# Performance work log

Measured on AMD Instinct MI355X. Metric: run time of the kernel, lower is better.

## Reference

```python
import jax, jax.numpy as jnp
import numpy as np

B, S, H = 64, 512, 768
BETA = 1.0
SENT_W, TOK_W, REG_W = 1.0, 1.0, 0.01


def setup_inputs() -> dict:
    key = jax.random.key(0)
    ks = jax.random.split(key, 8)
    hidden_states = jax.random.normal(ks[0], (B, S, H), dtype=jnp.float32)
    # offset_mapping[:,:,0] != 0 marks continuation subwords; position 0 is always a word start
    is_cont = jax.random.bernoulli(ks[1], 0.3, (B, S)).astype(jnp.int32)
    is_cont = is_cont.at[:, 0].set(0)
    offset_mapping = jnp.stack([is_cont, jnp.zeros((B, S), jnp.int32)], axis=-1)
    labels = jax.random.randint(ks[2], (B, S), 0, 2, dtype=jnp.int32)
    std = 0.02
    w1 = jax.random.normal(ks[3], (H, 100), jnp.float32) * std
    b1 = jnp.zeros((100,), jnp.float32)
    w2 = jax.random.normal(ks[4], (100, 1), jnp.float32) * std
    b2 = jnp.zeros((1,), jnp.float32)
    sw1 = jax.random.normal(ks[5], (H, 300), jnp.float32) * std
    sb1 = jnp.zeros((300,), jnp.float32)
    sw2 = jax.random.normal(ks[6], (300, 1), jnp.float32) * std
    sb2 = jnp.zeros((1,), jnp.float32)
    return dict(hidden_states=hidden_states, offset_mapping=offset_mapping, labels=labels,
                w1=w1, b1=b1, w2=w2, b2=b2, sw1=sw1, sb1=sb1, sw2=sw2, sb2=sb2)


def reference(hidden_states, offset_mapping, labels, w1, b1, w2, b2, sw1, sb1, sw2, sb2):
    b, s, h = hidden_states.shape
    # token attention head: Linear -> tanh -> Linear -> sigmoid, squeeze last dim
    tok = jax.nn.sigmoid(jnp.tanh(hidden_states @ w1 + b1) @ w2 + b2)[..., 0]  # [B,S]
    # vectorized segmented max over subword groups (replaces the python loop):
    # each word = a start position (offset[...,0]==0) plus following continuations.
    is_start = offset_mapping[:, :, 0] == 0  # [B,S]
    word_id = jnp.cumsum(is_start.astype(jnp.int32), axis=1) - 1  # per-row word index
    seg = (jnp.arange(b, dtype=jnp.int32)[:, None] * s + word_id).reshape(-1)  # global segment id
    segmax = jax.ops.segment_max(tok.reshape(-1), seg, num_segments=b * s)
    word_att = jnp.where(is_start, segmax[seg].reshape(b, s), tok)
    labf = labels.astype(tok.dtype)
    token_attention_mask = ((labels == 0) | (labels == 1)).astype(tok.dtype) * is_start.astype(tok.dtype)
    masked = word_att * token_attention_mask  # token_logits
    pw = jnp.power(masked, BETA)
    norm = pw / jnp.sum(pw, axis=1, keepdims=True)
    pooled = jnp.einsum('bsh,bs->bh', hidden_states, norm)  # bmm(hidden^T, att)
    sent = jax.nn.sigmoid(jnp.tanh(pooled @ sw1 + sb1) @ sw2 + sb2)  # [B,1] sequence_logits
    sentence_labels = jnp.max(labf, axis=1, keepdims=True)
    sentence_loss = jnp.sum((sent - sentence_labels) ** 2)
    zero_labels = jnp.where(labf == 1.0, labf, jnp.zeros_like(labf))
    token_loss = jnp.sum((masked - zero_labels) ** 2)
    ones_mask = jnp.where(masked == 0.0, jnp.ones_like(masked), masked)
    reg_a = jnp.sum(jnp.min(ones_mask, axis=1, keepdims=True) ** 2)
    reg_b = jnp.sum((jnp.max(masked, axis=1, keepdims=True) - sentence_labels) ** 2)
    loss = SENT_W * sentence_loss + TOK_W * token_loss + REG_W * (reg_a + reg_b)
    return loss, sentence_loss, token_loss, reg_a, reg_b, masked, sent
```

## Files before the change

kernel.cpp:

```cpp
#include <hip/hip_runtime.h>
#include <math.h>

#define BB   64
#define SS   512
#define HH   768
#define NU   100
#define NUP  112
#define NT   7
#define KS   24
#define NS1  300
#define MM   (BB*SS)
#define PCH  16
#define PTOK (SS/PCH)
#define UB   5
#define UPW  15

typedef __attribute__((ext_vector_type(8))) short short8;
typedef __attribute__((ext_vector_type(4))) float f32x4;

__device__ __forceinline__ unsigned short f2bf(float x) {
    unsigned int u = __float_as_uint(x);
    u = (u + 0x7FFFu + ((u >> 16) & 1u)) >> 16;
    return (unsigned short)u;
}

__device__ __forceinline__ float tanh_fast(float x) {
    float e = __expf(2.0f * x);
    return 1.0f - 2.0f / (e + 1.0f);
}

__device__ __forceinline__ float sigmoid_fast(float z) {
    return 1.0f / (1.0f + __expf(-z));
}

__global__ __launch_bounds__(64) void repack_kernel(
    const float* __restrict__ w1,
    const float* __restrict__ b1,
    const float* __restrict__ w2,
    const float* __restrict__ sw1,
    unsigned short* __restrict__ Bp,
    float* __restrict__ b1p, float* __restrict__ w2p,
    float* __restrict__ sw1T,
    float* __restrict__ accs,
    float* __restrict__ zacc,
    int*   __restrict__ btick)
{
    const int blk = blockIdx.x;
    const int l   = threadIdx.x;

    if (blk < NT * KS) {
        const int n  = blk / KS;
        const int ks = blk - n * KS;
        const int c  = l & 15, g = l >> 4;
        const int u  = n * 16 + c;

        unsigned int w[4];
#pragma unroll
        for (int jp = 0; jp < 4; jp++) {
            unsigned int lo, hi;
            {
                int k = ks * 32 + g * 8 + jp * 2;
                float x = (u < NU) ? w1[(size_t)k * NU + u] : 0.0f;
                lo = f2bf(x);
            }
            {
                int k = ks * 32 + g * 8 + jp * 2 + 1;
                float x = (u < NU) ? w1[(size_t)k * NU + u] : 0.0f;
                hi = f2bf(x);
            }
            w[jp] = lo | (hi << 16);
        }
        uint4* dst = (uint4*)(Bp + ((size_t)(n * KS + ks) * 64 + l) * 8);
        *dst = make_uint4(w[0], w[1], w[2], w[3]);

        if (blk == 0) {
            for (int i = l; i < NUP; i += 64) {
                b1p[i] = (i < NU) ? b1[i] : 0.0f;
                w2p[i] = (i < NU) ? w2[i] : 0.0f;
            }
            if (l < 8) accs[l] = 0.0f;
            zacc[l]  = 0.0f;
            btick[l] = 0;
        }
    } else {
        const int u = blk - NT * KS;
#pragma unroll
        for (int k = 0; k < HH / 64; k++) {
            int h = k * 64 + l;
            sw1T[(size_t)u * HH + h] = sw1[(size_t)h * NS1 + u];
        }
    }
}

__global__ __launch_bounds__(256) void tok_mlp_mfma(
    const float* __restrict__ hs,
    const unsigned short* __restrict__ Bp,
    const float* __restrict__ b1p,
    const float* __restrict__ w2p,
    const float* __restrict__ b2,
    float* __restrict__ tok)
{
    const int tid = threadIdx.x;
    const int wv = tid >> 6, l = tid & 63;
    const int c = l & 15, g = l >> 4;
    const int m0 = blockIdx.x * 64 + wv * 16;

    f32x4 acc[NT];
#pragma unroll
    for (int n = 0; n < NT; n++) acc[n] = (f32x4){0.f, 0.f, 0.f, 0.f};

    const float* arow = hs + (size_t)(m0 + c) * HH + g * 8;
    const unsigned short* bbase = Bp + (size_t)l * 8;

    float4 a0 = *(const float4*)(arow);
    float4 a1 = *(const float4*)(arow + 4);

    for (int ks = 0; ks < KS; ks++) {
        float4 n0 = a0, n1 = a1;
        if (ks + 1 < KS) {
            n0 = *(const float4*)(arow + (ks + 1) * 32);
            n1 = *(const float4*)(arow + (ks + 1) * 32 + 4);
        }
        short8 af;
        af[0] = (short)f2bf(a0.x); af[1] = (short)f2bf(a0.y);
        af[2] = (short)f2bf(a0.z); af[3] = (short)f2bf(a0.w);
        af[4] = (short)f2bf(a1.x); af[5] = (short)f2bf(a1.y);
        af[6] = (short)f2bf(a1.z); af[7] = (short)f2bf(a1.w);
#pragma unroll
        for (int n = 0; n < NT; n++) {
            short8 bf = *(const short8*)(bbase + (size_t)(n * KS + ks) * 64 * 8);
            acc[n] = __builtin_amdgcn_mfma_f32_16x16x32_bf16(af, bf, acc[n], 0, 0, 0);
        }
        a0 = n0; a1 = n1;
    }

    float p[4];
#pragma unroll
    for (int j = 0; j < 4; j++) {
        float s = 0.0f;
#pragma unroll
        for (int n = 0; n < NT; n++) {
            int u = n * 16 + c;
            s += tanh_fast(acc[n][j] + b1p[u]) * w2p[u];
        }
        p[j] = s;
    }
#pragma unroll
    for (int off = 1; off < 16; off <<= 1) {
#pragma unroll
        for (int j = 0; j < 4; j++) p[j] += __shfl_xor(p[j], off, 64);
    }
    if (c == 0) {
        float bias = b2[0];
#pragma unroll
        for (int j = 0; j < 4; j++) {
            float z = p[j] + bias;
            tok[m0 + g * 4 + j] = sigmoid_fast(z);
        }
    }
}

__global__ __launch_bounds__(256) void row_kernel(
    const float* __restrict__ tok,
    const int*   __restrict__ offset,
    const int*   __restrict__ labels,
    float* __restrict__ masked_out,
    float* __restrict__ rowsum,
    float* __restrict__ rowmax,
    float* __restrict__ rowmin,
    float* __restrict__ sentlab,
    float* __restrict__ accs)
{
    __shared__ float tokL[SS];
    __shared__ float maskedL[SS];
    __shared__ int   startL[SS];
    __shared__ int   labL[SS];
    __shared__ float wredA[4][5];

    const int b = blockIdx.x, tid = threadIdx.x;

    for (int s = tid; s < SS; s += 256) {
        tokL[s]   = tok[b * SS + s];
        startL[s] = (offset[(size_t)(b * SS + s) * 2] == 0) ? 1 : 0;
        labL[s]   = labels[b * SS + s];
    }
    __syncthreads();

    for (int s = tid; s < SS; s += 256) {
        float w;
        if (startL[s]) {
            float m = tokL[s];
            for (int j = s + 1; j < SS && !startL[j]; j++) m = fmaxf(m, tokL[j]);
            w = m;
        } else {
            w = tokL[s];
        }
        int lab = labL[s];
        float maskv = (((lab == 0) || (lab == 1)) && startL[s]) ? 1.0f : 0.0f;
        float mk = w * maskv;
        maskedL[s] = mk;
        masked_out[b * SS + s] = mk;
    }
    __syncthreads();

    float psum = 0.0f, pmax = -INFINITY, pmin = INFINITY, pml = 0.0f, ploss = 0.0f;
    for (int s = tid; s < SS; s += 256) {
        float mk = maskedL[s];
        psum += mk;
        pmax = fmaxf(pmax, mk);
        float ones = (mk == 0.0f) ? 1.0f : mk;
        pmin = fminf(pmin, ones);
        float lf = (float)labL[s];
        pml = fmaxf(pml, lf);
        float zl = (lf == 1.0f) ? lf : 0.0f;
        float d = mk - zl;
        ploss += d * d;
    }
#pragma unroll
    for (int off = 32; off >= 1; off >>= 1) {
        psum  += __shfl_xor(psum, off, 64);
        pmax   = fmaxf(pmax, __shfl_xor(pmax, off, 64));
        pmin   = fminf(pmin, __shfl_xor(pmin, off, 64));
        pml    = fmaxf(pml,  __shfl_xor(pml, off, 64));
        ploss += __shfl_xor(ploss, off, 64);
    }
    const int wv = tid >> 6, ln = tid & 63;
    if (ln == 0) {
        wredA[wv][0] = psum; wredA[wv][1] = pmax; wredA[wv][2] = pmin;
        wredA[wv][3] = pml;  wredA[wv][4] = ploss;
    }
    __syncthreads();
    if (tid == 0) {
        float s = 0.0f, mx = -INFINITY, mn = INFINITY, ml = 0.0f, ls = 0.0f;
        for (int w = 0; w < 4; w++) {
            s += wredA[w][0];
            mx = fmaxf(mx, wredA[w][1]);
            mn = fminf(mn, wredA[w][2]);
            ml = fmaxf(ml, wredA[w][3]);
            ls += wredA[w][4];
        }
        rowsum[b] = s; rowmax[b] = mx; rowmin[b] = mn; sentlab[b] = ml;
        atomicAdd(&accs[0], ls);
    }
}

__global__ __launch_bounds__(192) void pool_partial_kernel(
    const float* __restrict__ hs,
    const float* __restrict__ masked,
    const float* __restrict__ rowsum,
    float* __restrict__ pp)
{
    __shared__ float normL[PTOK];
    __shared__ float normC[PTOK];
    __shared__ int   idxC[PTOK];
    __shared__ int   cntS;
    const int b = blockIdx.x >> 4, p = blockIdx.x & 15;
    const int tid = threadIdx.x;
    const float inv = 1.0f / rowsum[b];
    if (tid < PTOK) normL[tid] = masked[b * SS + p * PTOK + tid] * inv;
    __syncthreads();
    if (tid == 0) {
        int c = 0;
        for (int s = 0; s < PTOK; s++) {
            float v = normL[s];
            if (v != 0.0f) { idxC[c] = s; normC[c] = v; c++; }
        }
        cntS = c;
    }
    __syncthreads();
    const int cnt = cntS;

    float4 a = make_float4(0.f, 0.f, 0.f, 0.f);
    const float* hb = hs + (size_t)b * SS * HH + (size_t)p * PTOK * HH;
#pragma unroll 2
    for (int i = 0; i < cnt; i++) {
        float w = normC[i];
        float4 v = *(const float4*)(hb + (size_t)idxC[i] * HH + tid * 4);
        a.x += v.x * w; a.y += v.y * w; a.z += v.z * w; a.w += v.w * w;
    }
    *(float4*)(pp + (size_t)(b * PCH + p) * HH + tid * 4) = a;
}

__global__ __launch_bounds__(256) void sent_kernel(
    const float* __restrict__ pp,
    const float* __restrict__ sw1T,
    const float* __restrict__ sb1,
    const float* __restrict__ sw2,
    const float* __restrict__ sb2,
    const float* __restrict__ rowmax,
    const float* __restrict__ rowmin,
    const float* __restrict__ sentlab,
    float* __restrict__ sent_out,
    float* __restrict__ accs,
    float* __restrict__ zacc,
    int*   __restrict__ btick,
    float* __restrict__ out)
{
    __shared__ float pooledL[HH];
    __shared__ float wzL[4];

    const int b = blockIdx.x / UB, ub = blockIdx.x - b * UB;
    const int tid = threadIdx.x;

    if (tid < 192) {
        float4 s = make_float4(0.f, 0.f, 0.f, 0.f);
        const float* base = pp + (size_t)b * PCH * HH + tid * 4;
#pragma unroll
        for (int p = 0; p < PCH; p++) {
            float4 v = *(const float4*)(base + (size_t)p * HH);
            s.x += v.x; s.y += v.y; s.z += v.z; s.w += v.w;
        }
        *(float4*)(&pooledL[tid * 4]) = s;
    }
    __syncthreads();

    const int wv = tid >> 6, l = tid & 63;
    float zp = 0.0f;
#pragma unroll
    for (int i = 0; i < UPW; i++) {
        const int u = ub * (4 * UPW) + wv * UPW + i;
        const float* r = sw1T + (size_t)u * HH;
        float s = 0.0f;
#pragma unroll
        for (int k = 0; k < 3; k++) {
            float4 v  = *(const float4*)(r + (k * 64 + l) * 4);
            float4 pv = *(const float4*)(&pooledL[(k * 64 + l) * 4]);
            s += v.x * pv.x + v.y * pv.y + v.z * pv.z + v.w * pv.w;
        }
#pragma unroll
        for (int off = 32; off >= 1; off >>= 1) s += __shfl_xor(s, off, 64);
        zp += tanh_fast(s + sb1[u]) * sw2[u];
    }
    if (l == 0) wzL[wv] = zp;
    __syncthreads();

    if (tid == 0) {
        float blockz = wzL[0] + wzL[1] + wzL[2] + wzL[3];
        atomicAdd(&zacc[b], blockz);
        __threadfence();
        int old = atomicAdd(&btick[b], 1);
        if (old == UB - 1) {
            float z = atomicAdd(&zacc[b], 0.0f) + sb2[0];
            float sentv = sigmoid_fast(z);
            sent_out[b] = sentv;
            float sl = sentlab[b];
            float ds = sentv - sl;
            atomicAdd(&accs[1], ds * ds);
            float dm = rowmax[b] - sl;
            atomicAdd(&accs[3], dm * dm);
            atomicAdd(&accs[2], rowmin[b] * rowmin[b]);
            __threadfence();
            int* t2 = (int*)(accs + 4);
            int o2 = atomicAdd(t2, 1);
            if (o2 == BB - 1) {
                float tokl  = atomicAdd(&accs[0], 0.0f);
                float sentl = atomicAdd(&accs[1], 0.0f);
                float rega  = atomicAdd(&accs[2], 0.0f);
                float regb  = atomicAdd(&accs[3], 0.0f);
                out[0] = sentl + tokl + 0.01f * (rega + regb);
                out[1] = sentl;
                out[2] = tokl;
                out[3] = rega;
                out[4] = regb;
            }
        }
    }
}

extern "C" void kernel_launch(void* const* d_in, const int* in_sizes, int n_in,
                              void* d_out, int out_size, void* d_ws, size_t ws_size,
                              hipStream_t stream)
{
    const float* hs     = (const float*)d_in[0];
    const int*   offm   = (const int*)  d_in[1];
    const int*   labels = (const int*)  d_in[2];
    const float* w1     = (const float*)d_in[3];
    const float* b1     = (const float*)d_in[4];
    const float* w2     = (const float*)d_in[5];
    const float* b2     = (const float*)d_in[6];
    const float* sw1    = (const float*)d_in[7];
    const float* sb1    = (const float*)d_in[8];
    const float* sw2    = (const float*)d_in[9];
    const float* sb2    = (const float*)d_in[10];

    float* out     = (float*)d_out;
    float* maskedO = out + 5;
    float* sentO   = out + 5 + MM;

    float* ws      = (float*)d_ws;
    float* tok     = ws;
    float* pp      = ws + MM;
    float* rowsum  = pp + (size_t)BB * PCH * HH;
    float* rowmax  = rowsum + BB;
    float* rowmin  = rowmax + BB;
    float* sentlab = rowmin + BB;
    float* accs    = sentlab + BB;
    float* zacc    = accs + 8;
    float* btickf  = zacc + BB;
    float* b1p     = btickf + BB;
    float* w2p     = b1p + NUP;
    float* sw1T    = w2p + NUP;
    size_t ofs = (size_t)((sw1T + (size_t)NS1 * HH) - ws);
    ofs = (ofs + 3) & ~(size_t)3;
    unsigned short* Bp = (unsigned short*)(ws + ofs);

    repack_kernel<<<NT * KS + NS1, 64, 0, stream>>>(w1, b1, w2, sw1, Bp, b1p, w2p,
                                                    sw1T, accs, zacc, (int*)btickf);
    tok_mlp_mfma<<<MM / 64, 256, 0, stream>>>(hs, Bp, b1p, w2p, b2, tok);
    row_kernel<<<BB, 256, 0, stream>>>(tok, offm, labels, maskedO,
                                       rowsum, rowmax, rowmin, sentlab, accs);
    pool_partial_kernel<<<BB * PCH, 192, 0, stream>>>(hs, maskedO, rowsum, pp);
    sent_kernel<<<BB * UB, 256, 0, stream>>>(pp, sw1T, sb1, sw2, sb2,
                                             rowmax, rowmin, sentlab, sentO,
                                             accs, zacc, (int*)btickf, out);
}
```

Measured before the change: 214.7 us.

## Stage packed token-MLP weights in shared memory with double buffering

Reorders the packed bf16 weight layout so each K-step slice is contiguous, then has the whole block cooperatively copy each slice into a double-buffered LDS tile before the MFMA loop reads it. This replaces per-wave global loads of the same weights by all four waves with one shared load per block. It also swaps the manual bf16 rounding for the packed hardware conversion intrinsic. In exchange it adds a block-wide barrier every K step, which may stall the loop.

After: 219.8 us. 1.02x slower.

```diff
diff --git a/kernel.cpp b/kernel.cpp
--- a/kernel.cpp
+++ b/kernel.cpp
@@ -1,4 +1,5 @@
 #include <hip/hip_runtime.h>
+#include <hip/hip_bf16.h>
 #include <math.h>
 
 #define BB   64
@@ -14,6 +15,7 @@
 #define PTOK (SS/PCH)
 #define UB   5
 #define UPW  15
+#define BSLOT (NT*64*8/8)
 
 typedef __attribute__((ext_vector_type(8))) short short8;
 typedef __attribute__((ext_vector_type(4))) float f32x4;
@@ -22,6 +24,11 @@
     unsigned int u = __float_as_uint(x);
     u = (u + 0x7FFFu + ((u >> 16) & 1u)) >> 16;
     return (unsigned short)u;
+}
+
+__device__ __forceinline__ unsigned int pk2(float lo, float hi) {
+    __hip_bfloat162 h = __float22bfloat162_rn(make_float2(lo, hi));
+    return *(unsigned int*)&h;
 }
 
 __device__ __forceinline__ float tanh_fast(float x) {
@@ -70,7 +77,7 @@
             }
             w[jp] = lo | (hi << 16);
         }
-        uint4* dst = (uint4*)(Bp + ((size_t)(n * KS + ks) * 64 + l) * 8);
+        uint4* dst = (uint4*)(Bp + ((size_t)(ks * NT + n) * 64 + l) * 8);
         *dst = make_uint4(w[0], w[1], w[2], w[3]);
 
         if (blk == 0) {
@@ -100,6 +107,8 @@
     const float* __restrict__ b2,
     float* __restrict__ tok)
 {
+    __shared__ __align__(16) unsigned short Bst[2][NT * 64 * 8];
+
     const int tid = threadIdx.x;
     const int wv = tid >> 6, l = tid & 63;
     const int c = l & 15, g = l >> 4;
@@ -110,10 +119,16 @@
     for (int n = 0; n < NT; n++) acc[n] = (f32x4){0.f, 0.f, 0.f, 0.f};
 
     const float* arow = hs + (size_t)(m0 + c) * HH + g * 8;
-    const unsigned short* bbase = Bp + (size_t)l * 8;
-
+    const uint4* bsrc = (const uint4*)Bp;
+
+    {
+        uint4* d = (uint4*)&Bst[0][0];
+        d[tid] = bsrc[tid];
+        if (tid + 256 < BSLOT) d[tid + 256] = bsrc[tid + 256];
+    }
     float4 a0 = *(const float4*)(arow);
     float4 a1 = *(const float4*)(arow + 4);
+    __syncthreads();
 
     for (int ks = 0; ks < KS; ks++) {
         float4 n0 = a0, n1 = a1;
@@ -121,16 +136,22 @@
             n0 = *(const float4*)(arow + (ks + 1) * 32);
             n1 = *(const float4*)(arow + (ks + 1) * 32 + 4);
         }
-        short8 af;
-        af[0] = (short)f2bf(a0.x); af[1] = (short)f2bf(a0.y);
-        af[2] = (short)f2bf(a0.z); af[3] = (short)f2bf(a0.w);
-        af[4] = (short)f2bf(a1.x); af[5] = (short)f2bf(a1.y);
-        af[6] = (short)f2bf(a1.z); af[7] = (short)f2bf(a1.w);
+        if (ks + 1 < KS) {
+            const uint4* s = bsrc + (size_t)(ks + 1) * BSLOT;
+            uint4* d = (uint4*)&Bst[(ks + 1) & 1][0];
+            d[tid] = s[tid];
+            if (tid + 256 < BSLOT) d[tid + 256] = s[tid + 256];
+        }
+        uint4 uu = make_uint4(pk2(a0.x, a0.y), pk2(a0.z, a0.w),
+                              pk2(a1.x, a1.y), pk2(a1.z, a1.w));
+        short8 af = *(short8*)&uu;
+        const unsigned short* bb = &Bst[ks & 1][l * 8];
 #pragma unroll
         for (int n = 0; n < NT; n++) {
-            short8 bf = *(const short8*)(bbase + (size_t)(n * KS + ks) * 64 * 8);
+            short8 bf = *(const short8*)(bb + n * 512);
             acc[n] = __builtin_amdgcn_mfma_f32_16x16x32_bf16(af, bf, acc[n], 0, 0, 0);
         }
+        __syncthreads();
         a0 = n0; a1 = n1;
     }
 
```

## Fuse token MLP with row reduction and pooling with sentence head via tickets

Applied to the files above, without the earlier changes.

Merges the token-MLP GEMM kernel with the per-row segmented max and reduction kernel. The last of the 8 blocks covering a row, found through an atomic ticket, does the row work. Pooling partials now accumulate into a pooled buffer with atomics, and the last of the 16 chunk blocks per row runs the sentence MLP, so the partial buffer and two launches go away. It also reorders the packed weight layout so each k-step reads contiguously, and uses packed bf16 conversion. The cost is that the row and sentence work runs serially in one block per row, and float atomic accumulation makes results nondeterministic.

Result: slower. 349.1 us (+62.6%).

```diff
diff --git a/kernel.cpp b/kernel.cpp
--- a/kernel.cpp
+++ b/kernel.cpp
@@ -1,4 +1,5 @@
 #include <hip/hip_runtime.h>
+#include <hip/hip_bf16.h>
 #include <math.h>
 
 #define BB   64
@@ -12,8 +13,6 @@
 #define MM   (BB*SS)
 #define PCH  16
 #define PTOK (SS/PCH)
-#define UB   5
-#define UPW  15
 
 typedef __attribute__((ext_vector_type(8))) short short8;
 typedef __attribute__((ext_vector_type(4))) float f32x4;
@@ -22,6 +21,15 @@
     unsigned int u = __float_as_uint(x);
     u = (u + 0x7FFFu + ((u >> 16) & 1u)) >> 16;
     return (unsigned short)u;
+}
+
+__device__ __forceinline__ unsigned int pk2(float lo, float hi) {
+    __hip_bfloat162 h = __float22bfloat162_rn(make_float2(lo, hi));
+    return *(unsigned int*)&h;
+}
+
+__device__ __forceinline__ float aload(const float* p) {
+    return __hip_atomic_load(p, __ATOMIC_RELAXED, __HIP_MEMORY_SCOPE_AGENT);
 }
 
 __device__ __forceinline__ float tanh_fast(float x) {
@@ -42,8 +50,9 @@
     float* __restrict__ b1p, float* __restrict__ w2p,
     float* __restrict__ sw1T,
     float* __restrict__ accs,
-    float* __restrict__ zacc,
-    int*   __restrict__ btick)
+    float* __restrict__ pooled,
+    int*   __restrict__ rowdone,
+    int*   __restrict__ pticket)
 {
     const int blk = blockIdx.x;
     const int l   = threadIdx.x;
@@ -70,7 +79,7 @@
             }
             w[jp] = lo | (hi << 16);
         }
-        uint4* dst = (uint4*)(Bp + ((size_t)(n * KS + ks) * 64 + l) * 8);
+        uint4* dst = (uint4*)(Bp + ((size_t)(ks * NT + n) * 64 + l) * 8);
         *dst = make_uint4(w[0], w[1], w[2], w[3]);
 
         if (blk == 0) {
@@ -79,96 +88,37 @@
                 w2p[i] = (i < NU) ? w2[i] : 0.0f;
             }
             if (l < 8) accs[l] = 0.0f;
-            zacc[l]  = 0.0f;
-            btick[l] = 0;
-        }
-    } else {
+        }
+    } else if (blk < NT * KS + NS1) {
         const int u = blk - NT * KS;
 #pragma unroll
         for (int k = 0; k < HH / 64; k++) {
             int h = k * 64 + l;
             sw1T[(size_t)u * HH + h] = sw1[(size_t)h * NS1 + u];
         }
-    }
-}
-
-__global__ __launch_bounds__(256) void tok_mlp_mfma(
+    } else {
+        const int b = blk - (NT * KS + NS1);
+        float4 z4 = make_float4(0.f, 0.f, 0.f, 0.f);
+#pragma unroll
+        for (int k = 0; k < 3; k++)
+            *(float4*)(pooled + (size_t)b * HH + (k * 64 + l) * 4) = z4;
+        if (l == 0) { rowdone[b] = 0; pticket[b] = 0; }
+    }
+}
+
+__global__ __launch_bounds__(256) void tok_row_kernel(
     const float* __restrict__ hs,
     const unsigned short* __restrict__ Bp,
     const float* __restrict__ b1p,
     const float* __restrict__ w2p,
-    const float* __restrict__ b2,
-    float* __restrict__ tok)
-{
-    const int tid = threadIdx.x;
-    const int wv = tid >> 6, l = tid & 63;
-    const int c = l & 15, g = l >> 4;
-    const int m0 = blockIdx.x * 64 + wv * 16;
-
-    f32x4 acc[NT];
-#pragma unroll
-    for (int n = 0; n < NT; n++) acc[n] = (f32x4){0.f, 0.f, 0.f, 0.f};
-
-    const float* arow = hs + (size_t)(m0 + c) * HH + g * 8;
-    const unsigned short* bbase = Bp + (size_t)l * 8;
-
-    float4 a0 = *(const float4*)(arow);
-    float4 a1 = *(const float4*)(arow + 4);
-
-    for (int ks = 0; ks < KS; ks++) {
-        float4 n0 = a0, n1 = a1;
-        if (ks + 1 < KS) {
-            n0 = *(const float4*)(arow + (ks + 1) * 32);
-            n1 = *(const float4*)(arow + (ks + 1) * 32 + 4);
-        }
-        short8 af;
-        af[0] = (short)f2bf(a0.x); af[1] = (short)f2bf(a0.y);
-        af[2] = (short)f2bf(a0.z); af[3] = (short)f2bf(a0.w);
-        af[4] = (short)f2bf(a1.x); af[5] = (short)f2bf(a1.y);
-        af[6] = (short)f2bf(a1.z); af[7] = (short)f2bf(a1.w);
-#pragma unroll
-        for (int n = 0; n < NT; n++) {
-            short8 bf = *(const short8*)(bbase + (size_t)(n * KS + ks) * 64 * 8);
-            acc[n] = __builtin_amdgcn_mfma_f32_16x16x32_bf16(af, bf, acc[n], 0, 0, 0);
-        }
-        a0 = n0; a1 = n1;
-    }
-
-    float p[4];
-#pragma unroll
-    for (int j = 0; j < 4; j++) {
-        float s = 0.0f;
-#pragma unroll
-        for (int n = 0; n < NT; n++) {
-            int u = n * 16 + c;
-            s += tanh_fast(acc[n][j] + b1p[u]) * w2p[u];
-        }
-        p[j] = s;
-    }
-#pragma unroll
-    for (int off = 1; off < 16; off <<= 1) {
-#pragma unroll
-        for (int j = 0; j < 4; j++) p[j] += __shfl_xor(p[j], off, 64);
-    }
-    if (c == 0) {
-        float bias = b2[0];
-#pragma unroll
-        for (int j = 0; j < 4; j++) {
-            float z = p[j] + bias;
-            tok[m0 + g * 4 + j] = sigmoid_fast(z);
-        }
-    }
-}
-
-__global__ __launch_bounds__(256) void row_kernel(
-    const float* __restrict__ tok,
+    const float* __restrict__ b2g,
     const int*   __restrict__ offset,
     const int*   __restrict__ labels,
+    float* __restrict__ tokg,
     float* __restrict__ masked_out,
-    float* __restrict__ rowsum,
-    float* __restrict__ rowmax,
-    float* __restrict__ rowmin,
-    float* __restrict__ sentlab,
+    float* __restrict__ rowsum, float* __restrict__ rowmax,
+    float* __restrict__ rowmin, float* __restrict__ sentlab,
+    int*   __restrict__ rowdone,
     float* __restrict__ accs)
 {
     __shared__ float tokL[SS];
@@ -176,13 +126,80 @@
     __shared__ int   startL[SS];
     __shared__ int   labL[SS];
     __shared__ float wredA[4][5];
-
-    const int b = blockIdx.x, tid = threadIdx.x;
+    __shared__ int   isLast;
+
+    const int tid = threadIdx.x;
+    const int wv = tid >> 6, l = tid & 63;
+    const int c = l & 15, g = l >> 4;
+    const int m0 = blockIdx.x * 64 + wv * 16;
+    const int brow = blockIdx.x >> 3;
+
+    f32x4 acc[NT];
+#pragma unroll
+    for (int n = 0; n < NT; n++) acc[n] = (f32x4){0.f, 0.f, 0.f, 0.f};
+
+    const float* arow = hs + (size_t)(m0 + c) * HH + g * 8;
+    const unsigned short* bbase = Bp + (size_t)l * 8;
+
+    float4 a0 = *(const float4*)(arow);
+    float4 a1 = *(const float4*)(arow + 4);
+
+    for (int ks = 0; ks < KS; ks++) {
+        float4 n0 = a0, n1 = a1;
+        if (ks + 1 < KS) {
+            n0 = *(const float4*)(arow + (ks + 1) * 32);
+            n1 = *(const float4*)(arow + (ks + 1) * 32 + 4);
+        }
+        uint4 uu = make_uint4(pk2(a0.x, a0.y), pk2(a0.z, a0.w),
+                              pk2(a1.x, a1.y), pk2(a1.z, a1.w));
+        short8 af = *(short8*)&uu;
+#pragma unroll
+        for (int n = 0; n < NT; n++) {
+            short8 bf = *(const short8*)(bbase + (size_t)(ks * NT + n) * 512);
+            acc[n] = __builtin_amdgcn_mfma_f32_16x16x32_bf16(af, bf, acc[n], 0, 0, 0);
+        }
+        a0 = n0; a1 = n1;
+    }
+
+    float p[4];
+#pragma unroll
+    for (int j = 0; j < 4; j++) {
+        float s = 0.0f;
+#pragma unroll
+        for (int n = 0; n < NT; n++) {
+            int u = n * 16 + c;
+            s += tanh_fast(acc[n][j] + b1p[u]) * w2p[u];
+        }
+        p[j] = s;
+    }
+#pragma unroll
+    for (int off = 1; off < 16; off <<= 1) {
+#pragma unroll
+        for (int j = 0; j < 4; j++) p[j] += __shfl_xor(p[j], off, 64);
+    }
+    if (c == 0) {
+        float bias = b2g[0];
+#pragma unroll
+        for (int j = 0; j < 4; j++) {
+            float z = p[j] + bias;
+            tokg[m0 + g * 4 + j] = sigmoid_fast(z);
+        }
+    }
+
+    __syncthreads();
+    if (tid == 0) {
+        __threadfence();
+        int old = atomicAdd(&rowdone[brow], 1);
+        isLast = (old == 7) ? 1 : 0;
+    }
+    __syncthreads();
+    if (!isLast) return;
+    __threadfence();
 
     for (int s = tid; s < SS; s += 256) {
-        tokL[s]   = tok[b * SS + s];
-        startL[s] = (offset[(size_t)(b * SS + s) * 2] == 0) ? 1 : 0;
-        labL[s]   = labels[b * SS + s];
+        tokL[s]   = aload(&tokg[brow * SS + s]);
+        startL[s] = (offset[(size_t)(brow * SS + s) * 2] == 0) ? 1 : 0;
+        labL[s]   = labels[brow * SS + s];
     }
     __syncthreads();
 
@@ -199,7 +216,7 @@
         float maskv = (((lab == 0) || (lab == 1)) && startL[s]) ? 1.0f : 0.0f;
         float mk = w * maskv;
         maskedL[s] = mk;
-        masked_out[b * SS + s] = mk;
+        masked_out[brow * SS + s] = mk;
     }
     __syncthreads();
 
@@ -224,8 +241,7 @@
         pml    = fmaxf(pml,  __shfl_xor(pml, off, 64));
         ploss += __shfl_xor(ploss, off, 64);
     }
-    const int wv = tid >> 6, ln = tid & 63;
-    if (ln == 0) {
+    if (l == 0) {
         wredA[wv][0] = psum; wredA[wv][1] = pmax; wredA[wv][2] = pmin;
         wredA[wv][3] = pml;  wredA[wv][4] = ploss;
     }
@@ -239,50 +255,15 @@
             ml = fmaxf(ml, wredA[w][3]);
             ls += wredA[w][4];
         }
-        rowsum[b] = s; rowmax[b] = mx; rowmin[b] = mn; sentlab[b] = ml;
+        rowsum[brow] = s; rowmax[brow] = mx; rowmin[brow] = mn; sentlab[brow] = ml;
         atomicAdd(&accs[0], ls);
     }
 }
 
-__global__ __launch_bounds__(192) void pool_partial_kernel(
+__global__ __launch_bounds__(384) void pool_sent_kernel(
     const float* __restrict__ hs,
     const float* __restrict__ masked,
     const float* __restrict__ rowsum,
-    float* __restrict__ pp)
-{
-    __shared__ float normL[PTOK];
-    __shared__ float normC[PTOK];
-    __shared__ int   idxC[PTOK];
-    __shared__ int   cntS;
-    const int b = blockIdx.x >> 4, p = blockIdx.x & 15;
-    const int tid = threadIdx.x;
-    const float inv = 1.0f / rowsum[b];
-    if (tid < PTOK) normL[tid] = masked[b * SS + p * PTOK + tid] * inv;
-    __syncthreads();
-    if (tid == 0) {
-        int c = 0;
-        for (int s = 0; s < PTOK; s++) {
-            float v = normL[s];
-            if (v != 0.0f) { idxC[c] = s; normC[c] = v; c++; }
-        }
-        cntS = c;
-    }
-    __syncthreads();
-    const int cnt = cntS;
-
-    float4 a = make_float4(0.f, 0.f, 0.f, 0.f);
-    const float* hb = hs + (size_t)b * SS * HH + (size_t)p * PTOK * HH;
-#pragma unroll 2
-    for (int i = 0; i < cnt; i++) {
-        float w = normC[i];
-        float4 v = *(const float4*)(hb + (size_t)idxC[i] * HH + tid * 4);
-        a.x += v.x * w; a.y += v.y * w; a.z += v.z * w; a.w += v.w * w;
-    }
-    *(float4*)(pp + (size_t)(b * PCH + p) * HH + tid * 4) = a;
-}
-
-__global__ __launch_bounds__(256) void sent_kernel(
-    const float* __restrict__ pp,
     const float* __restrict__ sw1T,
     const float* __restrict__ sb1,
     const float* __restrict__ sw2,
@@ -290,35 +271,67 @@
     const float* __restrict__ rowmax,
     const float* __restrict__ rowmin,
     const float* __restrict__ sentlab,
+    float* __restrict__ pooled,
+    int*   __restrict__ pticket,
     float* __restrict__ sent_out,
     float* __restrict__ accs,
-    float* __restrict__ zacc,
-    int*   __restrict__ btick,
     float* __restrict__ out)
 {
+    __shared__ float normL[PTOK];
+    __shared__ float normC[PTOK];
+    __shared__ int   idxC[PTOK];
+    __shared__ int   cntS;
+    __shared__ int   isLast;
     __shared__ float pooledL[HH];
-    __shared__ float wzL[4];
-
-    const int b = blockIdx.x / UB, ub = blockIdx.x - b * UB;
+    __shared__ float wzL[6];
+
+    const int b = blockIdx.x >> 4, p = blockIdx.x & 15;
     const int tid = threadIdx.x;
 
-    if (tid < 192) {
-        float4 s = make_float4(0.f, 0.f, 0.f, 0.f);
-        const float* base = pp + (size_t)b * PCH * HH + tid * 4;
-#pragma unroll
-        for (int p = 0; p < PCH; p++) {
-            float4 v = *(const float4*)(base + (size_t)p * HH);
-            s.x += v.x; s.y += v.y; s.z += v.z; s.w += v.w;
-        }
-        *(float4*)(&pooledL[tid * 4]) = s;
-    }
+    const float inv = 1.0f / rowsum[b];
+    if (tid < PTOK) normL[tid] = masked[b * SS + p * PTOK + tid] * inv;
+    __syncthreads();
+    if (tid == 0) {
+        int c = 0;
+        for (int s = 0; s < PTOK; s++) {
+            float v = normL[s];
+            if (v != 0.0f) { idxC[c] = s; normC[c] = v; c++; }
+        }
+        cntS = c;
+    }
+    __syncthreads();
+    const int cnt = cntS;
+
+    float ax = 0.0f, ay = 0.0f;
+    const float* hb = hs + (size_t)b * SS * HH + (size_t)p * PTOK * HH;
+#pragma unroll 2
+    for (int i = 0; i < cnt; i++) {
+        float w = normC[i];
+        float2 v = *(const float2*)(hb + (size_t)idxC[i] * HH + tid * 2);
+        ax += v.x * w; ay += v.y * w;
+    }
+    atomicAdd(&pooled[(size_t)b * HH + tid * 2],     ax);
+    atomicAdd(&pooled[(size_t)b * HH + tid * 2 + 1], ay);
+
+    __syncthreads();
+    if (tid == 0) {
+        __threadfence();
+        int old = atomicAdd(&pticket[b], 1);
+        isLast = (old == PCH - 1) ? 1 : 0;
+    }
+    __syncthreads();
+    if (!isLast) return;
+    __threadfence();
+
+    pooledL[tid]       = aload(&pooled[(size_t)b * HH + tid]);
+    pooledL[tid + 384] = aload(&pooled[(size_t)b * HH + tid + 384]);
     __syncthreads();
 
     const int wv = tid >> 6, l = tid & 63;
     float zp = 0.0f;
 #pragma unroll
-    for (int i = 0; i < UPW; i++) {
-        const int u = ub * (4 * UPW) + wv * UPW + i;
+    for (int i = 0; i < 50; i++) {
+        const int u = wv * 50 + i;
         const float* r = sw1T + (size_t)u * HH;
         float s = 0.0f;
 #pragma unroll
@@ -335,34 +348,29 @@
     __syncthreads();
 
     if (tid == 0) {
-        float blockz = wzL[0] + wzL[1] + wzL[2] + wzL[3];
-        atomicAdd(&zacc[b], blockz);
+        float z = wzL[0] + wzL[1] + wzL[2] + wzL[3] + wzL[4] + wzL[5] + sb2[0];
+        float sentv = sigmoid_fast(z);
+        sent_out[b] = sentv;
+        float sl = sentlab[b];
+        float ds = sentv - sl;
+        atomicAdd(&accs[1], ds * ds);
+        float dm = rowmax[b] - sl;
+        atomicAdd(&accs[3], dm * dm);
+        atomicAdd(&accs[2], rowmin[b] * rowmin[b]);
+
         __threadfence();
-        int old = atomicAdd(&btick[b], 1);
-        if (old == UB - 1) {
-            float z = atomicAdd(&zacc[b], 0.0f) + sb2[0];
-            float sentv = sigmoid_fast(z);
-            sent_out[b] = sentv;
-            float sl = sentlab[b];
-            float ds = sentv - sl;
-            atomicAdd(&accs[1], ds * ds);
-            float dm = rowmax[b] - sl;
-            atomicAdd(&accs[3], dm * dm);
-            atomicAdd(&accs[2], rowmin[b] * rowmin[b]);
-            __threadfence();
-            int* t2 = (int*)(accs + 4);
-            int o2 = atomicAdd(t2, 1);
-            if (o2 == BB - 1) {
-                float tokl  = atomicAdd(&accs[0], 0.0f);
-                float sentl = atomicAdd(&accs[1], 0.0f);
-                float rega  = atomicAdd(&accs[2], 0.0f);
-                float regb  = atomicAdd(&accs[3], 0.0f);
-                out[0] = sentl + tokl + 0.01f * (rega + regb);
-                out[1] = sentl;
-                out[2] = tokl;
-                out[3] = rega;
-                out[4] = regb;
-            }
+        int* t2 = (int*)(accs + 4);
+        int o2 = atomicAdd(t2, 1);
+        if (o2 == BB - 1) {
+            float tokl  = atomicAdd(&accs[0], 0.0f);
+            float sentl = atomicAdd(&accs[1], 0.0f);
+            float rega  = atomicAdd(&accs[2], 0.0f);
+            float regb  = atomicAdd(&accs[3], 0.0f);
+            out[0] = sentl + tokl + 0.01f * (rega + regb);
+            out[1] = sentl;
+            out[2] = tokl;
+            out[3] = rega;
+            out[4] = regb;
         }
     }
 }
@@ -389,28 +397,28 @@
 
     float* ws      = (float*)d_ws;
     float* tok     = ws;
-    float* pp      = ws + MM;
-    float* rowsum  = pp + (size_t)BB * PCH * HH;
+    float* rowsum  = tok + MM;
     float* rowmax  = rowsum + BB;
     float* rowmin  = rowmax + BB;
     float* sentlab = rowmin + BB;
     float* accs    = sentlab + BB;
-    float* zacc    = accs + 8;
-    float* btickf  = zacc + BB;
-    float* b1p     = btickf + BB;
+    float* rowdf   = accs + 8;
+    float* ptickf  = rowdf + BB;
+    float* pooled  = ptickf + BB;
+    float* b1p     = pooled + (size_t)BB * HH;
     float* w2p     = b1p + NUP;
     float* sw1T    = w2p + NUP;
     size_t ofs = (size_t)((sw1T + (size_t)NS1 * HH) - ws);
     ofs = (ofs + 3) & ~(size_t)3;
     unsigned short* Bp = (unsigned short*)(ws + ofs);
 
-    repack_kernel<<<NT * KS + NS1, 64, 0, stream>>>(w1, b1, w2, sw1, Bp, b1p, w2p,
-                                                    sw1T, accs, zacc, (int*)btickf);
-    tok_mlp_mfma<<<MM / 64, 256, 0, stream>>>(hs, Bp, b1p, w2p, b2, tok);
-    row_kernel<<<BB, 256, 0, stream>>>(tok, offm, labels, maskedO,
-                                       rowsum, rowmax, rowmin, sentlab, accs);
-    pool_partial_kernel<<<BB * PCH, 192, 0, stream>>>(hs, maskedO, rowsum, pp);
-    sent_kernel<<<BB * UB, 256, 0, stream>>>(pp, sw1T, sb1, sw2, sb2,
-                                             rowmax, rowmin, sentlab, sentO,
-                                             accs, zacc, (int*)btickf, out);
-}
+    repack_kernel<<<NT * KS + NS1 + BB, 64, 0, stream>>>(
+        w1, b1, w2, sw1, Bp, b1p, w2p, sw1T, accs, pooled,
+        (int*)rowdf, (int*)ptickf);
+    tok_row_kernel<<<MM / 64, 256, 0, stream>>>(
+        hs, Bp, b1p, w2p, b2, offm, labels, tok, maskedO,
+        rowsum, rowmax, rowmin, sentlab, (int*)rowdf, accs);
+    pool_sent_kernel<<<BB * PCH, 384, 0, stream>>>(
+        hs, maskedO, rowsum, sw1T, sb1, sw2, sb2,
+        rowmax, rowmin, sentlab, pooled, (int*)ptickf, sentO, accs, out);
+}
```
